# Performance work log

Measured on AMD Instinct MI355X. Metric: run time of the kernel, lower is better.

## Reference

```python
import jax, jax.numpy as jnp
import numpy as np

B, S, E, H, DK = 4, 1024, 1024, 16, 64
FF = 2048
SCALE = int(np.sqrt(DK))  # source uses int(np.sqrt(keySize)) = 8
EPS = 1e-5


def _mha(x_kv, x_q, Wq, Wk, Wv, Wo, mask):
    # Wq/Wk/Wv: [H, E, DK]; Wo: [H*DK, E]
    k = jnp.einsum('bse,hed->hbsd', x_kv, Wk)   # [H,B,S,DK]
    v = jnp.einsum('bse,hed->hbsd', x_kv, Wv)
    q = jnp.einsum('bse,hed->hbsd', x_q, Wq)
    # source does keys.reshape(B, DK, S) -- a RAW reshape, not a transpose
    kR = k.reshape(H, B, DK, S)
    scores = jnp.einsum('hbsd,hbdt->hbst', q, kR)  # [H,B,S,S]
    if mask is not None:
        scores = scores + mask  # mask added BEFORE the scale divide, as in source
    att = jax.nn.softmax(scores / SCALE, axis=-1)
    out = jnp.einsum('hbst,hbtd->hbsd', att, v)    # [H,B,S,DK]
    # source stacks heads then does a RAW reshape [H,B,S,DK] -> [B,S,DK*H]
    out = out.reshape(B, S, DK * H)
    return out @ Wo  # [B,S,E]


def _layernorm2d(x, w, b):
    # LayerNorm over last two dims (S, E) with affine params [S, E]
    m = jnp.mean(x, axis=(-2, -1), keepdims=True)
    v = jnp.var(x, axis=(-2, -1), keepdims=True)
    return (x - m) * jax.lax.rsqrt(v + EPS) * w + b


def setup_inputs() -> dict:
    key = jax.random.key(0)
    ks = jax.random.split(key, 24)
    u = lambda k, shp: jax.random.uniform(k, shp, dtype=jnp.float32)  # weights ~ U(0,1) as in source
    inp = {
        'inputRes': jax.random.normal(ks[0], (B, S, E), dtype=jnp.float32),
        'outputEncoding': jax.random.normal(ks[1], (B, S, E), dtype=jnp.float32),
        'Wq1': u(ks[2], (H, E, DK)), 'Wk1': u(ks[3], (H, E, DK)), 'Wv1': u(ks[4], (H, E, DK)),
        'Wo1': u(ks[5], (H * DK, E)),
        'Wq2': u(ks[6], (H, E, DK)), 'Wk2': u(ks[7], (H, E, DK)), 'Wv2': u(ks[8], (H, E, DK)),
        'Wo2': u(ks[9], (H * DK, E)),
        'ln1_w': jnp.ones((S, E), jnp.float32), 'ln1_b': jnp.zeros((S, E), jnp.float32),
        'ln2_w': jnp.ones((S, E), jnp.float32), 'ln2_b': jnp.zeros((S, E), jnp.float32),
        'ln3_w': jnp.ones((S, E), jnp.float32), 'ln3_b': jnp.zeros((S, E), jnp.float32),
        'W1': jax.random.normal(ks[10], (S, FF), dtype=jnp.float32) * (1.0 / np.sqrt(S)),
        'b1': jnp.zeros((FF,), jnp.float32),
        'W2': jax.random.normal(ks[11], (FF, S), dtype=jnp.float32) * (1.0 / np.sqrt(FF)),
        'b2': jnp.zeros((S,), jnp.float32),
    }
    return inp


def reference(inputRes, outputEncoding, Wq1, Wk1, Wv1, Wo1, Wq2, Wk2, Wv2, Wo2,
              ln1_w, ln1_b, ln2_w, ln2_b, ln3_w, ln3_b, W1, b1, W2, b2):
    # causal mask: row i has 0 for j<=i, -inf for j>i
    idx = jnp.arange(S)
    mask = jnp.where(idx[None, :] <= idx[:, None], 0.0, -jnp.inf).astype(jnp.float32)

    # masked self-attention + residual + LN1
    att = _mha(outputEncoding, outputEncoding, Wq1, Wk1, Wv1, Wo1, mask)
    att_norm = _layernorm2d(att + outputEncoding, ln1_w, ln1_b)

    # cross-attention (K,V from inputRes; Q from att_norm) + residual to outputEncoding + LN2
    att2 = _mha(inputRes, att_norm, Wq2, Wk2, Wv2, Wo2, None)
    att2_norm = _layernorm2d(att2 + outputEncoding, ln2_w, ln2_b)

    # FFN over the sequence dim via RAW reshape (B,S,E)->(B,E,S), as in source
    norm_res = att2_norm.reshape(B, E, S)
    fc = jax.nn.relu(norm_res @ W1 + b1) @ W2 + b2  # [B,E,S]
    fc = fc.reshape(B, S, E)

    return _layernorm2d(fc + att2_norm, ln3_w, ln3_b)
```

## Files before the change

kernel.cpp:

```cpp
#include <hip/hip_runtime.h>
#include <cstdint>
#include <cstddef>


#define DI __device__ __forceinline__
#define MFMA __builtin_amdgcn_mfma_f32_16x16x32_bf16

typedef short s8v __attribute__((ext_vector_type(8)));
typedef float f4v __attribute__((ext_vector_type(4)));
typedef unsigned u4v __attribute__((ext_vector_type(4)));

DI float bf2f(short u){
  union { unsigned int i; float f; } v;
  v.i = ((unsigned int)(unsigned short)u) << 16;
  return v.f;
}
DI short f2bf(float f){
  union { float f; unsigned int i; } v; v.f = f;
  unsigned int x = v.i;
  return (short)((x + 0x7fffu + ((x >> 16) & 1u)) >> 16);
}
DI unsigned pack2(short hi, short lo){
  return ((unsigned)(unsigned short)lo << 16) | (unsigned)(unsigned short)hi;
}
DI unsigned packf(float val){
  short hi = f2bf(val);
  return pack2(hi, f2bf(val - bf2f(hi)));
}
DI void gload16(const void* g, void* l){
  __builtin_amdgcn_global_load_lds(
      (const __attribute__((address_space(1))) unsigned*)g,
      (__attribute__((address_space(3))) unsigned*)l, 16, 0, 0);
}

struct SplitP { const float* src[2]; short* hi[2]; short* lo[2]; };

__launch_bounds__(256)
__global__ void splitall_k(SplitP sp){
  const int t = blockIdx.y;
  int i = (blockIdx.x * 256 + threadIdx.x) << 2;
  float4 v = *(const float4*)(sp.src[t] + i);
  float xs[4] = {v.x, v.y, v.z, v.w};
  short h[4], l[4];
  #pragma unroll
  for (int c = 0; c < 4; c++){
    h[c] = f2bf(xs[c]);
    l[c] = f2bf(xs[c] - bf2f(h[c]));
  }
  *(short4*)(sp.hi[t] + i) = make_short4(h[0], h[1], h[2], h[3]);
  *(short4*)(sp.lo[t] + i) = make_short4(l[0], l[1], l[2], l[3]);
}

struct TransP {
  const float* src[10];
  short* oh[10]; short* ol[10];
  int Kd[10]; int Nd[10]; int qkv[10]; int ntiles[10];
};

__launch_bounds__(256)
__global__ void transall_k(TransP tp){
  const int t = blockIdx.y;
  const int tile = blockIdx.x;
  if (tile >= tp.ntiles[t]) return;
  const int K = tp.Kd[t], N = tp.Nd[t];
  const int ncols = N >> 6;
  const int n0 = (tile % ncols) << 6, k0 = (tile / ncols) << 6;
  __shared__ float Ld[64 * 65];
  const int tid = threadIdx.x;
  const int row = tid >> 2, c16 = (tid & 3) << 4;
  const float* s = tp.src[t];
  size_t base;
  if (tp.qkv[t]) base = ((size_t)(n0 >> 6) << 16) + ((size_t)(k0 + row) << 6) + c16;
  else           base = (size_t)(k0 + row) * N + n0 + c16;
  #pragma unroll
  for (int j4 = 0; j4 < 4; j4++){
    float4 v = *(const float4*)(s + base + (j4 << 2));
    int c = row * 65 + c16 + (j4 << 2);
    Ld[c] = v.x; Ld[c + 1] = v.y; Ld[c + 2] = v.z; Ld[c + 3] = v.w;
  }
  __syncthreads();
  const int n = tid >> 2;
  s8v h0, h1, l0, l1;
  #pragma unroll
  for (int j = 0; j < 8; j++){
    float a = Ld[(c16 + j) * 65 + n];
    float b = Ld[(c16 + 8 + j) * 65 + n];
    short ha = f2bf(a), hb = f2bf(b);
    h0[j] = ha; l0[j] = f2bf(a - bf2f(ha));
    h1[j] = hb; l1[j] = f2bf(b - bf2f(hb));
  }
  size_t ob = (size_t)(n0 + n) * K + k0 + c16;
  *(s8v*)(tp.oh[t] + ob)     = h0;
  *(s8v*)(tp.oh[t] + ob + 8) = h1;
  *(s8v*)(tp.ol[t] + ob)     = l0;
  *(s8v*)(tp.ol[t] + ob + 8) = l1;
}

struct GemmP {
  const short* Ah; const short* Al; int lda;
  const short* Bh; const short* Bl; int ldb;
  int K; int N;
  const float* xres; const float* bias;
  float* outf;
  short* o1h; short* o1l;
  unsigned* p1; unsigned* p2; unsigned* p3;
};

template<int TM, int EPI, int TERMS>
__launch_bounds__(512, 2)
__global__ void gemm_k(GemmP p){
  constexpr int NG = (TERMS == 3) ? (TM / 64 + 2) : (TM / 128 + 2);
  constexpr int WM = TM >> 6;
  constexpr int NB = 128 / (8 / WM) / 16;
  __shared__ short AhL[3][TM * 32];
  __shared__ short AlL[3][(TERMS == 3) ? TM * 32 : 8];
  __shared__ short BhL[3][128 * 32];
  __shared__ short BlL[3][128 * 32];
  const int tid = threadIdx.x;
  const int L = tid & 63, w = tid >> 6;
  const int lr = L & 15, lg = L >> 4;
  const int mo = (w & (WM - 1)) << 6;
  const int no = (w / WM) * (NB << 4);

  const int gx = gridDim.x, gy = gridDim.y;
  const int f = blockIdx.y * gx + blockIdx.x;
  const int j = f >> 3;
  const int jm = j / gx;
  const int mb = (f & 7) * (gy >> 3) + jm;
  const int nb = j - jm * gx;
  const int m0 = mb * TM, n0 = nb << 7;

  const int lrow4 = L >> 2, lq = L & 3;

  int aoff[4], boff[NB];
  #pragma unroll
  for (int mi = 0; mi < 4; mi++){
    int r = mo + (mi << 4) + lr;
    aoff[mi] = (r << 5) + ((lg ^ ((r >> 1) & 3)) << 3);
  }
  #pragma unroll
  for (int ni = 0; ni < NB; ni++){
    int n = no + (ni << 4) + lr;
    boff[ni] = (n << 5) + ((lg ^ ((n >> 1) & 3)) << 3);
  }

  f4v acc[4][NB];
  #pragma unroll
  for (int i = 0; i < 4; i++)
    #pragma unroll
    for (int jj = 0; jj < NB; jj++)
      #pragma unroll
      for (int r = 0; r < 4; r++) acc[i][jj][r] = 0.0f;

  const int nkt = p.K >> 5;

  auto stage1 = [&](int tile, int slot, int i){
    const int k0 = tile << 5;
    int base_c = (i << 9) + (w << 6);
    const short* plane; short* lds; int row0; int ld; int pc;
    if (base_c < TM * 4){
      pc = base_c; plane = p.Ah; lds = &AhL[slot][0]; row0 = m0; ld = p.lda;
    } else if (TERMS == 3 && base_c < TM * 8){
      pc = base_c - TM * 4; plane = p.Al; lds = &AlL[slot][0]; row0 = m0; ld = p.lda;
    } else {
      int pc2 = base_c - (TERMS == 3 ? TM * 8 : TM * 4);
      if (pc2 < 512){ pc = pc2; plane = p.Bh; lds = &BhL[slot][0]; }
      else          { pc = pc2 - 512; plane = p.Bl; lds = &BlL[slot][0]; }
      row0 = n0; ld = p.ldb;
    }
    int rl = (pc >> 2) + lrow4;
    int sc = (lq ^ ((rl >> 1) & 3)) << 3;
    gload16(plane + (size_t)(row0 + rl) * ld + k0 + sc, lds + (pc << 3));
  };

  #pragma unroll
  for (int i = 0; i < NG; i++) stage1(0, 0, i);
  #pragma unroll
  for (int i = 0; i < NG; i++) stage1(1, 1, i);

  for (int kt = 0; kt < nkt; kt++){
    const int cur = kt % 3;
    const int nt = kt + 2 < nkt ? kt + 2 : nkt - 1;
    const int nslot = (kt + 2) % 3;
    asm volatile("s_waitcnt vmcnt(%0)\n\ts_barrier" :: "i"(NG) : "memory");

    s8v a_h[4], b_h[NB];
    #pragma unroll
    for (int mi = 0; mi < 4; mi++) a_h[mi] = *(const s8v*)&AhL[cur][aoff[mi]];
    #pragma unroll
    for (int ni = 0; ni < NB; ni++) b_h[ni] = *(const s8v*)&BhL[cur][boff[ni]];
    stage1(nt, nslot, 0);
    stage1(nt, nslot, 1);
    __builtin_amdgcn_s_barrier();
    __builtin_amdgcn_s_setprio(1);
    #pragma unroll
    for (int ni = 0; ni < NB; ni++)
      #pragma unroll
      for (int mi = 0; mi < 4; mi++)
        acc[mi][ni] = MFMA(a_h[mi], b_h[ni], acc[mi][ni], 0, 0, 0);
    __builtin_amdgcn_s_setprio(0);
    __builtin_amdgcn_s_barrier();

    s8v b_l[NB];
    #pragma unroll
    for (int ni = 0; ni < NB; ni++) b_l[ni] = *(const s8v*)&BlL[cur][boff[ni]];
    if (NG > 2) stage1(nt, nslot, 2);
    if (NG > 3) stage1(nt, nslot, 3);
    __builtin_amdgcn_s_barrier();
    __builtin_amdgcn_s_setprio(1);
    #pragma unroll
    for (int ni = 0; ni < NB; ni++)
      #pragma unroll
      for (int mi = 0; mi < 4; mi++)
        acc[mi][ni] = MFMA(a_h[mi], b_l[ni], acc[mi][ni], 0, 0, 0);
    __builtin_amdgcn_s_setprio(0);

    if (TERMS == 3){
      __builtin_amdgcn_s_barrier();
      s8v a_l[4];
      #pragma unroll
      for (int mi = 0; mi < 4; mi++) a_l[mi] = *(const s8v*)&AlL[cur][aoff[mi]];
      if (NG > 4) stage1(nt, nslot, 4);
      if (NG > 5) stage1(nt, nslot, 5);
      __builtin_amdgcn_s_barrier();
      __builtin_amdgcn_s_setprio(1);
      #pragma unroll
      for (int ni = 0; ni < NB; ni++)
        #pragma unroll
        for (int mi = 0; mi < 4; mi++)
          acc[mi][ni] = MFMA(a_l[mi], b_h[ni], acc[mi][ni], 0, 0, 0);
      __builtin_amdgcn_s_setprio(0);
    }
  }

  #pragma unroll
  for (int mi = 0; mi < 4; mi++){
    #pragma unroll
    for (int ni = 0; ni < NB; ni++){
      #pragma unroll
      for (int r = 0; r < 4; r++){
        float val = acc[mi][ni][r];
        int m = m0 + mo + (mi << 4) + (lg << 2) + r;
        int n = n0 + no + (ni << 4) + lr;
        if (EPI == 2){
          size_t o = (size_t)m * p.N + n;
          p.outf[o] = val + p.xres[o];
        } else if (EPI == 4){
          p.outf[(size_t)m * p.N + n] = val + p.bias[n];
        } else if (EPI == 3){
          float x = val + p.bias[n];
          x = x > 0.0f ? x : 0.0f;
          size_t o = (size_t)m * p.N + n;
          short hi = f2bf(x);
          p.o1h[o] = hi;
          p.o1l[o] = f2bf(x - bf2f(hi));
        } else {
          int seg = (EPI == 0) ? 0 : (n >> 10);
          int n1 = (EPI == 0) ? n : (n & 1023);
          int kind = (EPI == 0) ? 0 : (EPI == 6 ? seg : seg + 1);
          int b = m >> 10, s = m & 1023, hh = n1 >> 6, d = n1 & 63;
          size_t hb16 = (size_t)((hh << 2) | b) << 16;
          size_t dst;
          if (kind == 0)      dst = hb16 + ((size_t)s << 6) + d;
          else if (kind == 1) dst = hb16 + ((size_t)(((s & 15) << 6) | d) << 6) + (s >> 4);
          else                dst = hb16 + ((size_t)d << 10) + s;
          unsigned* dp = (EPI == 0) ? p.p1
                       : (EPI == 6) ? (seg == 0 ? p.p1 : (seg == 1 ? p.p2 : p.p3))
                                    : (seg == 0 ? p.p1 : p.p2);
          dp[dst] = packf(val);
        }
      }
    }
  }
}

template<int CAUSAL>
__launch_bounds__(256, 2)
__global__ void flash_k(const unsigned* __restrict__ qpk,
                        const unsigned* __restrict__ kpk,
                        const unsigned* __restrict__ vpk,
                        short* __restrict__ ohi_g, short* __restrict__ olo_g){
  __shared__ short Kt[2][64*72];
  __shared__ short Vt[2][64*72];
  __shared__ unsigned Ps[2][4][16*68];
  const int tid = threadIdx.x, L = tid & 63, w = tid >> 6;
  const int lr = L & 15, lg = L >> 4;
  const int flat = blockIdx.x + (blockIdx.y << 3);
  const int hb = ((flat & 7) << 3) | ((flat >> 3) & 7);
  const int sp = flat >> 6;
  const int h = hb >> 2, b = hb & 3;
  const size_t hbo = (size_t)hb << 16;
  const float NEG_INF = -__builtin_inff();
  int qt[2]; qt[0] = sp; qt[1] = CAUSAL ? (15 - sp) : (sp + 8);

  s8v qfh[2][2], qfl[2][2];
  #pragma unroll
  for (int st = 0; st < 2; st++){
    const unsigned* qg = qpk + hbo + (size_t)((qt[st] << 6) + (w << 4) + lr) * 64 + (lg << 3);
    #pragma unroll
    for (int ks = 0; ks < 2; ks++){
      u4v p0 = *(const u4v*)(qg + (ks << 5));
      u4v p1 = *(const u4v*)(qg + (ks << 5) + 4);
      #pragma unroll
      for (int jj = 0; jj < 4; jj++){
        qfh[st][ks][jj]     = (short)(p0[jj] & 0xffffu);
        qfl[st][ks][jj]     = (short)(p0[jj] >> 16);
        qfh[st][ks][4 + jj] = (short)(p1[jj] & 0xffffu);
        qfl[st][ks][4 + jj] = (short)(p1[jj] >> 16);
      }
    }
  }

  f4v o[2][4];
  float mprev[2][4], lsum[2][4];
  #pragma unroll
  for (int st = 0; st < 2; st++){
    #pragma unroll
    for (int ni = 0; ni < 4; ni++)
      #pragma unroll
      for (int r = 0; r < 4; r++) o[st][ni][r] = 0.0f;
    #pragma unroll
    for (int r = 0; r < 4; r++){ mprev[st][r] = NEG_INF; lsum[st][r] = 0.0f; }
  }

  const int ntt = CAUSAL ? (qt[1] + 1) : 16;
  for (int ti = 0; ti < ntt; ti++){
    const int t0 = ti << 6;
    const bool actA = !(CAUSAL && ti > qt[0]);
    __syncthreads();
    {
      const int row = tid >> 2, col = (tid & 3) << 4;
      const unsigned* kg = kpk + hbo + (size_t)(t0 + row) * 64 + col;
      const unsigned* vg = vpk + hbo + ((size_t)row << 10) + t0 + col;
      unsigned kb[16], vb[16];
      #pragma unroll
      for (int j4 = 0; j4 < 4; j4++){
        *(u4v*)&kb[j4 << 2] = *(const u4v*)(kg + (j4 << 2));
        *(u4v*)&vb[j4 << 2] = *(const u4v*)(vg + (j4 << 2));
      }
      s8v kh0, kh1, kl0, kl1, vh0, vh1, vl0, vl1;
      #pragma unroll
      for (int jj = 0; jj < 8; jj++){
        kh0[jj] = (short)(kb[jj] & 0xffffu);      kl0[jj] = (short)(kb[jj] >> 16);
        kh1[jj] = (short)(kb[8 + jj] & 0xffffu);  kl1[jj] = (short)(kb[8 + jj] >> 16);
        vh0[jj] = (short)(vb[jj] & 0xffffu);      vl0[jj] = (short)(vb[jj] >> 16);
        vh1[jj] = (short)(vb[8 + jj] & 0xffffu);  vl1[jj] = (short)(vb[8 + jj] >> 16);
      }
      const int lb = row * 72 + col;
      *(s8v*)&Kt[0][lb] = kh0;  *(s8v*)&Kt[0][lb + 8] = kh1;
      *(s8v*)&Kt[1][lb] = kl0;  *(s8v*)&Kt[1][lb + 8] = kl1;
      *(s8v*)&Vt[0][lb] = vh0;  *(s8v*)&Vt[0][lb + 8] = vh1;
      *(s8v*)&Vt[1][lb] = vl0;  *(s8v*)&Vt[1][lb + 8] = vl1;
    }
    __syncthreads();

    f4v sa[2][4];
    #pragma unroll
    for (int st = 0; st < 2; st++)
      #pragma unroll
      for (int ni = 0; ni < 4; ni++)
        #pragma unroll
        for (int r = 0; r < 4; r++) sa[st][ni][r] = 0.0f;
    #pragma unroll
    for (int ks = 0; ks < 2; ks++){
      const int kb = (ks << 5) + (lg << 3);
      #pragma unroll
      for (int ni = 0; ni < 4; ni++){
        const int tl = (ni << 4) + lr;
        s8v kbh = *(const s8v*)&Kt[0][tl * 72 + kb];
        s8v kbl = *(const s8v*)&Kt[1][tl * 72 + kb];
        if (actA){
          sa[0][ni] = MFMA(qfh[0][ks], kbh, sa[0][ni], 0, 0, 0);
          sa[0][ni] = MFMA(qfh[0][ks], kbl, sa[0][ni], 0, 0, 0);
          sa[0][ni] = MFMA(qfl[0][ks], kbh, sa[0][ni], 0, 0, 0);
        }
        sa[1][ni] = MFMA(qfh[1][ks], kbh, sa[1][ni], 0, 0, 0);
        sa[1][ni] = MFMA(qfh[1][ks], kbl, sa[1][ni], 0, 0, 0);
        sa[1][ni] = MFMA(qfl[1][ks], kbh, sa[1][ni], 0, 0, 0);
      }
    }

    #pragma unroll
    for (int st = 0; st < 2; st++){
      if (st == 0 && !actA) continue;
      const int s0w = (qt[st] << 6) + (w << 4);
      const bool diag = CAUSAL && (ti == qt[st]);
      float tm[4] = {NEG_INF, NEG_INF, NEG_INF, NEG_INF};
      #pragma unroll
      for (int ni = 0; ni < 4; ni++)
        #pragma unroll
        for (int r = 0; r < 4; r++){
          float v = sa[st][ni][r] * 0.125f;
          if (diag){
            int tg = t0 + (ni << 4) + lr;
            int sg = s0w + (lg << 2) + r;
            if (tg > sg) v = NEG_INF;
          }
          sa[st][ni][r] = v;
          tm[r] = fmaxf(tm[r], v);
        }
      #pragma unroll
      for (int off = 1; off < 16; off <<= 1)
        #pragma unroll
        for (int r = 0; r < 4; r++) tm[r] = fmaxf(tm[r], __shfl_xor(tm[r], off, 16));
      float alpha[4], psum[4];
      #pragma unroll
      for (int r = 0; r < 4; r++){
        float mn = fmaxf(mprev[st][r], tm[r]);
        alpha[r] = __expf(mprev[st][r] - mn);
        mprev[st][r] = mn;
        psum[r] = 0.0f;
      }
      #pragma unroll
      for (int ni = 0; ni < 4; ni++)
        #pragma unroll
        for (int r = 0; r < 4; r++){
          float pv = __expf(sa[st][ni][r] - mprev[st][r]);
          sa[st][ni][r] = pv;
          psum[r] += pv;
        }
      #pragma unroll
      for (int off = 1; off < 16; off <<= 1)
        #pragma unroll
        for (int r = 0; r < 4; r++) psum[r] += __shfl_xor(psum[r], off, 16);
      #pragma unroll
      for (int r = 0; r < 4; r++) lsum[st][r] = lsum[st][r] * alpha[r] + psum[r];
      #pragma unroll
      for (int ni = 0; ni < 4; ni++)
        #pragma unroll
        for (int r = 0; r < 4; r++) o[st][ni][r] *= alpha[r];
      #pragma unroll
      for (int ni = 0; ni < 4; ni++)
        #pragma unroll
        for (int r = 0; r < 4; r++){
          int prow = (lg << 2) + r, pcol = (ni << 4) + lr;
          Ps[st][w][prow * 68 + pcol] = packf(sa[st][ni][r]);
        }
    }

    #pragma unroll
    for (int ks = 0; ks < 2; ks++){
      const int kb = (ks << 5) + (lg << 3);
      s8v ph[2], pl[2];
      #pragma unroll
      for (int st = 0; st < 2; st++){
        if (st == 0 && !actA) continue;
        u4v p0 = *(const u4v*)&Ps[st][w][lr * 68 + kb];
        u4v p1 = *(const u4v*)&Ps[st][w][lr * 68 + kb + 4];
        #pragma unroll
        for (int jj = 0; jj < 4; jj++){
          ph[st][jj]     = (short)(p0[jj] & 0xffffu);  pl[st][jj]     = (short)(p0[jj] >> 16);
          ph[st][4 + jj] = (short)(p1[jj] & 0xffffu);  pl[st][4 + jj] = (short)(p1[jj] >> 16);
        }
      }
      #pragma unroll
      for (int ni = 0; ni < 4; ni++){
        const int d = (ni << 4) + lr;
        s8v vbh = *(const s8v*)&Vt[0][d * 72 + kb];
        s8v vbl = *(const s8v*)&Vt[1][d * 72 + kb];
        if (actA){
          o[0][ni] = MFMA(ph[0], vbh, o[0][ni], 0, 0, 0);
          o[0][ni] = MFMA(ph[0], vbl, o[0][ni], 0, 0, 0);
          o[0][ni] = MFMA(pl[0], vbh, o[0][ni], 0, 0, 0);
        }
        o[1][ni] = MFMA(ph[1], vbh, o[1][ni], 0, 0, 0);
        o[1][ni] = MFMA(ph[1], vbl, o[1][ni], 0, 0, 0);
        o[1][ni] = MFMA(pl[1], vbh, o[1][ni], 0, 0, 0);
      }
    }
  }

  #pragma unroll
  for (int st = 0; st < 2; st++){
    const int s0w = (qt[st] << 6) + (w << 4);
    #pragma unroll
    for (int ni = 0; ni < 4; ni++){
      #pragma unroll
      for (int r = 0; r < 4; r++){
        float val = o[st][ni][r] / lsum[st][r];
        int s = s0w + (lg << 2) + r;
        int d = (ni << 4) + lr;
        int s2i = ((h & 3) << 8) | (b << 6) | (s >> 4);
        int c   = ((s & 15) << 6) | d;
        size_t dst = ((size_t)(h >> 2) << 20) + ((size_t)s2i << 10) + c;
        short hi = f2bf(val);
        ohi_g[dst] = hi;
        olo_g[dst] = f2bf(val - bf2f(hi));
      }
    }
  }
}

__launch_bounds__(256)
__global__ void ln_partial_k(const float* s1, const float* s2, float2* part){
  const int tid = threadIdx.x, L = tid & 63, w = tid >> 6;
  const int b = blockIdx.y, j = blockIdx.x;
  const size_t base = ((size_t)b << 20) + ((size_t)j << 13) + ((size_t)tid << 2);
  float sum = 0.0f, ss = 0.0f;
  #pragma unroll
  for (int i = 0; i < 8; i++){
    size_t idx = base + ((size_t)i << 10);
    float4 v = *(const float4*)(s1 + idx);
    if (s2){
      float4 u = *(const float4*)(s2 + idx);
      v.x += u.x; v.y += u.y; v.z += u.z; v.w += u.w;
    }
    sum += v.x + v.y + v.z + v.w;
    ss  += v.x*v.x + v.y*v.y + v.z*v.z + v.w*v.w;
  }
  #pragma unroll
  for (int off = 1; off < 64; off <<= 1){
    sum += __shfl_xor(sum, off, 64);
    ss  += __shfl_xor(ss,  off, 64);
  }
  __shared__ float red[4][2];
  if (L == 0){ red[w][0] = sum; red[w][1] = ss; }
  __syncthreads();
  if (tid == 0){
    float s_ = red[0][0] + red[1][0] + red[2][0] + red[3][0];
    float q_ = red[0][1] + red[1][1] + red[2][1] + red[3][1];
    part[b * 128 + j] = make_float2(s_, q_);
  }
}

__launch_bounds__(64)
__global__ void ln_final_k(const float2* part, float2* stats){
  const int b = blockIdx.x, t = threadIdx.x;
  float2 a = part[b * 128 + t], c = part[b * 128 + 64 + t];
  float sum = a.x + c.x, ss = a.y + c.y;
  #pragma unroll
  for (int off = 1; off < 64; off <<= 1){
    sum += __shfl_xor(sum, off, 64);
    ss  += __shfl_xor(ss,  off, 64);
  }
  if (t == 0){
    float mean = sum * (1.0f / 1048576.0f);
    float var  = ss  * (1.0f / 1048576.0f) - mean * mean;
    stats[b] = make_float2(mean, rsqrtf(var + 1e-5f));
  }
}

template<int MODE>
__launch_bounds__(256)
__global__ void ln_apply_k(const float* s1, const float* s2,
                           const float* wgt, const float* bias,
                           const float2* stats,
                           float* dstf, short* dsta, short* dstb){
  const int tid = threadIdx.x;
  const size_t base = ((size_t)blockIdx.x << 11) + ((size_t)tid << 2);
  #pragma unroll
  for (int i = 0; i < 2; i++){
    size_t idx = base + ((size_t)i << 10);
    int b = (int)(idx >> 20);
    float2 st = stats[b];
    float4 x = *(const float4*)(s1 + idx);
    if (s2){
      float4 u = *(const float4*)(s2 + idx);
      x.x += u.x; x.y += u.y; x.z += u.z; x.w += u.w;
    }
    unsigned wi = (unsigned)(idx & 1048575u);
    float4 wv = *(const float4*)(wgt + wi);
    float4 bv = *(const float4*)(bias + wi);
    float xv[4] = {x.x, x.y, x.z, x.w};
    float wvv[4] = {wv.x, wv.y, wv.z, wv.w};
    float bvv[4] = {bv.x, bv.y, bv.z, bv.w};
    float yv[4];
    #pragma unroll
    for (int c = 0; c < 4; c++)
      yv[c] = (xv[c] - st.x) * st.y * wvv[c] + bvv[c];
    if (MODE == 0 || MODE == 1){
      short h[4], l[4];
      #pragma unroll
      for (int c = 0; c < 4; c++){
        h[c] = f2bf(yv[c]);
        l[c] = f2bf(yv[c] - bf2f(h[c]));
      }
      *(short4*)(dsta + idx) = make_short4(h[0], h[1], h[2], h[3]);
      *(short4*)(dstb + idx) = make_short4(l[0], l[1], l[2], l[3]);
      if (MODE == 1)
        *(float4*)(dstf + idx) = make_float4(yv[0], yv[1], yv[2], yv[3]);
    } else {
      *(float4*)(dstf + idx) = make_float4(yv[0], yv[1], yv[2], yv[3]);
    }
  }
}

extern "C" void kernel_launch(void* const* d_in, const int* in_sizes, int n_in,
                              void* d_out, int out_size, void* d_ws, size_t ws_size,
                              hipStream_t stream){
  const float* IRf = (const float*)d_in[0];
  const float* OEf = (const float*)d_in[1];
  const float* Wq1f = (const float*)d_in[2];
  const float* Wk1f = (const float*)d_in[3];
  const float* Wv1f = (const float*)d_in[4];
  const float* Wo1f = (const float*)d_in[5];
  const float* Wq2f = (const float*)d_in[6];
  const float* Wk2f = (const float*)d_in[7];
  const float* Wv2f = (const float*)d_in[8];
  const float* Wo2f = (const float*)d_in[9];
  const float* ln1w = (const float*)d_in[10];
  const float* ln1b = (const float*)d_in[11];
  const float* ln2w = (const float*)d_in[12];
  const float* ln2b = (const float*)d_in[13];
  const float* ln3w = (const float*)d_in[14];
  const float* ln3b = (const float*)d_in[15];
  const float* W1f = (const float*)d_in[16];
  const float* b1f = (const float*)d_in[17];
  const float* W2f = (const float*)d_in[18];
  const float* b2f = (const float*)d_in[19];
  float* dout = (float*)d_out;

  char* ws = (char*)d_ws;
  const size_t MB = (size_t)1 << 20;
  short* OEh = (short*)(ws + 0*MB),  *OEl = (short*)(ws + 8*MB);
  short* IRh = (short*)(ws + 16*MB), *IRl = (short*)(ws + 24*MB);
  short* QKV1t_h = (short*)(ws + 32*MB), *QKV1t_l = (short*)(ws + 38*MB);
  short* Wo1t_h  = (short*)(ws + 44*MB), *Wo1t_l  = (short*)(ws + 46*MB);
  short* Q2t_h   = (short*)(ws + 48*MB), *Q2t_l   = (short*)(ws + 50*MB);
  short* KV2t_h  = (short*)(ws + 52*MB), *KV2t_l  = (short*)(ws + 56*MB);
  short* Wo2t_h  = (short*)(ws + 60*MB), *Wo2t_l  = (short*)(ws + 62*MB);
  short* W1t_h   = (short*)(ws + 64*MB), *W1t_l   = (short*)(ws + 68*MB);
  short* W2t_h   = (short*)(ws + 72*MB), *W2t_l   = (short*)(ws + 76*MB);
  unsigned* q_pk = (unsigned*)(ws + 80*MB);
  unsigned* k_pk = (unsigned*)(ws + 96*MB);
  unsigned* v_pk = (unsigned*)(ws + 112*MB);
  short* outr_h = (short*)(ws + 128*MB), *outr_l = (short*)(ws + 136*MB);
  float* resid = (float*)(ws + 144*MB);
  short* attn_h = (short*)(ws + 160*MB), *attn_l = (short*)(ws + 168*MB);
  float* att2n_f = (float*)(ws + 176*MB);
  short* hid_h = (short*)(ws + 80*MB);
  short* hid_l = (short*)(ws + 96*MB);
  float* fc    = (float*)(ws + 112*MB);
  short* a2n_h = (short*)(ws + 160*MB);
  short* a2n_l = (short*)(ws + 168*MB);
  float2* part  = (float2*)(ws + 192*MB);
  float2* stats = (float2*)(ws + 192*MB + 65536);

  dim3 blk(256), blkg(512);

  SplitP sp;
  sp.src[0] = OEf; sp.hi[0] = OEh; sp.lo[0] = OEl;
  sp.src[1] = IRf; sp.hi[1] = IRh; sp.lo[1] = IRl;
  splitall_k<<<dim3(4096, 2), blk, 0, stream>>>(sp);

  TransP tp;
  const float* tsrc[10] = {Wq1f, Wk1f, Wv1f, Wo1f, Wq2f, Wk2f, Wv2f, Wo2f, W1f, W2f};
  short* toh[10] = {QKV1t_h, QKV1t_h + (1<<20), QKV1t_h + (2<<20), Wo1t_h,
                    Q2t_h, KV2t_h, KV2t_h + (1<<20), Wo2t_h, W1t_h, W2t_h};
  short* tol[10] = {QKV1t_l, QKV1t_l + (1<<20), QKV1t_l + (2<<20), Wo1t_l,
                    Q2t_l, KV2t_l, KV2t_l + (1<<20), Wo2t_l, W1t_l, W2t_l};
  int tK[10]   = {1024,1024,1024,1024,1024,1024,1024,1024,1024,2048};
  int tN[10]   = {1024,1024,1024,1024,1024,1024,1024,1024,2048,1024};
  int tq[10]   = {1,1,1,0,1,1,1,0,0,0};
  int tt[10]   = {256,256,256,256,256,256,256,256,512,512};
  for (int i = 0; i < 10; i++){
    tp.src[i] = tsrc[i]; tp.oh[i] = toh[i]; tp.ol[i] = tol[i];
    tp.Kd[i] = tK[i]; tp.Nd[i] = tN[i]; tp.qkv[i] = tq[i]; tp.ntiles[i] = tt[i];
  }
  transall_k<<<dim3(512, 10), blk, 0, stream>>>(tp);

  GemmP p{};

  p = {OEh, OEl, 1024, QKV1t_h, QKV1t_l, 1024, 1024, 3072, nullptr, nullptr,
       nullptr, nullptr, nullptr, q_pk, k_pk, v_pk};
  gemm_k<256,6,3><<<dim3(24, 16), blkg, 0, stream>>>(p);
  flash_k<1><<<dim3(8, 64), blk, 0, stream>>>(q_pk, k_pk, v_pk, outr_h, outr_l);
  p = {outr_h, outr_l, 1024, Wo1t_h, Wo1t_l, 1024, 1024, 1024, OEf, nullptr,
       resid, nullptr, nullptr, nullptr, nullptr, nullptr};
  gemm_k<128,2,3><<<dim3(8, 32), blkg, 0, stream>>>(p);
  ln_partial_k<<<dim3(128, 4), blk, 0, stream>>>(resid, nullptr, part);
  ln_final_k<<<dim3(4), dim3(64), 0, stream>>>(part, stats);
  ln_apply_k<0><<<dim3(2048), blk, 0, stream>>>(resid, nullptr, ln1w, ln1b, stats, nullptr, attn_h, attn_l);

  p = {attn_h, attn_l, 1024, Q2t_h, Q2t_l, 1024, 1024, 1024, nullptr, nullptr,
       nullptr, nullptr, nullptr, q_pk, nullptr, nullptr};
  gemm_k<128,0,3><<<dim3(8, 32), blkg, 0, stream>>>(p);
  p = {IRh, IRl, 1024, KV2t_h, KV2t_l, 1024, 1024, 2048, nullptr, nullptr,
       nullptr, nullptr, nullptr, k_pk, v_pk, nullptr};
  gemm_k<256,7,3><<<dim3(16, 16), blkg, 0, stream>>>(p);
  flash_k<0><<<dim3(8, 64), blk, 0, stream>>>(q_pk, k_pk, v_pk, outr_h, outr_l);
  p = {outr_h, outr_l, 1024, Wo2t_h, Wo2t_l, 1024, 1024, 1024, OEf, nullptr,
       resid, nullptr, nullptr, nullptr, nullptr, nullptr};
  gemm_k<128,2,3><<<dim3(8, 32), blkg, 0, stream>>>(p);
  ln_partial_k<<<dim3(128, 4), blk, 0, stream>>>(resid, nullptr, part);
  ln_final_k<<<dim3(4), dim3(64), 0, stream>>>(part, stats);
  ln_apply_k<1><<<dim3(2048), blk, 0, stream>>>(resid, nullptr, ln2w, ln2b, stats, att2n_f, a2n_h, a2n_l);

  p = {a2n_h, a2n_l, 1024, W1t_h, W1t_l, 1024, 1024, 2048, nullptr, b1f,
       nullptr, hid_h, hid_l, nullptr, nullptr, nullptr};
  gemm_k<256,3,2><<<dim3(16, 16), blkg, 0, stream>>>(p);
  p = {hid_h, hid_l, 2048, W2t_h, W2t_l, 2048, 2048, 1024, nullptr, b2f,
       fc, nullptr, nullptr, nullptr, nullptr, nullptr};
  gemm_k<128,4,2><<<dim3(8, 32), blkg, 0, stream>>>(p);
  ln_partial_k<<<dim3(128, 4), blk, 0, stream>>>(fc, att2n_f, part);
  ln_final_k<<<dim3(4), dim3(64), 0, stream>>>(part, stats);
  ln_apply_k<2><<<dim3(2048), blk, 0, stream>>>(fc, att2n_f, ln3w, ln3b, stats, dout, nullptr, nullptr);
}
```

Before: 738.6 us.

## Restructure split-bf16 GEMM pipeline: double-buffer hi planes, stream Bl from registers

The GEMM main loop drops from a three-stage LDS ring holding all four hi/lo planes to a two-stage ring for only the hi planes. The B low plane now loads straight from global memory into registers, and the A low plane sits in a single-buffered LDS tile refilled after a barrier. The Bh·Al and Al·Bh MFMAs are interleaved, and per-phase barriers and setprio calls are removed. The smaller LDS footprint lets launch bounds rise to 4 blocks per CU, and two GEMMs switch from 256-row to 128-row tiles with doubled grids. The trade-offs are less prefetch depth, uncoalesced direct-to-register Bl loads, and extra register pressure under the tighter occupancy bound.

Measured after the change: 903.6 us. +22.3%, slower.

```diff
diff --git a/kernel.cpp b/kernel.cpp
--- a/kernel.cpp
+++ b/kernel.cpp
@@ -107,15 +107,15 @@
 };
 
 template<int TM, int EPI, int TERMS>
-__launch_bounds__(512, 2)
+__launch_bounds__(512, 4)
 __global__ void gemm_k(GemmP p){
-  constexpr int NG = (TERMS == 3) ? (TM / 64 + 2) : (TM / 128 + 2);
   constexpr int WM = TM >> 6;
   constexpr int NB = 128 / (8 / WM) / 16;
-  __shared__ short AhL[3][TM * 32];
-  __shared__ short AlL[3][(TERMS == 3) ? TM * 32 : 8];
-  __shared__ short BhL[3][128 * 32];
-  __shared__ short BlL[3][128 * 32];
+  constexpr int NH = TM / 128 + 1;
+  constexpr int NA = (TERMS == 3) ? TM / 128 : 0;
+  __shared__ short AhL[2][TM * 32];
+  __shared__ short BhL[2][128 * 32];
+  __shared__ short AlL[(TERMS == 3) ? TM * 32 : 8];
   const int tid = threadIdx.x;
   const int L = tid & 63, w = tid >> 6;
   const int lr = L & 15, lg = L >> 4;
@@ -154,83 +154,82 @@
 
   const int nkt = p.K >> 5;
 
-  auto stage1 = [&](int tile, int slot, int i){
+  auto stage_hi = [&](int tile, int slot, int i){
     const int k0 = tile << 5;
     int base_c = (i << 9) + (w << 6);
     const short* plane; short* lds; int row0; int ld; int pc;
     if (base_c < TM * 4){
       pc = base_c; plane = p.Ah; lds = &AhL[slot][0]; row0 = m0; ld = p.lda;
-    } else if (TERMS == 3 && base_c < TM * 8){
-      pc = base_c - TM * 4; plane = p.Al; lds = &AlL[slot][0]; row0 = m0; ld = p.lda;
     } else {
-      int pc2 = base_c - (TERMS == 3 ? TM * 8 : TM * 4);
-      if (pc2 < 512){ pc = pc2; plane = p.Bh; lds = &BhL[slot][0]; }
-      else          { pc = pc2 - 512; plane = p.Bl; lds = &BlL[slot][0]; }
-      row0 = n0; ld = p.ldb;
+      pc = base_c - TM * 4; plane = p.Bh; lds = &BhL[slot][0]; row0 = n0; ld = p.ldb;
     }
     int rl = (pc >> 2) + lrow4;
     int sc = (lq ^ ((rl >> 1) & 3)) << 3;
     gload16(plane + (size_t)(row0 + rl) * ld + k0 + sc, lds + (pc << 3));
   };
-
-  #pragma unroll
-  for (int i = 0; i < NG; i++) stage1(0, 0, i);
-  #pragma unroll
-  for (int i = 0; i < NG; i++) stage1(1, 1, i);
+  auto stage_al = [&](int tile, int i){
+    const int k0 = tile << 5;
+    int pc = (i << 9) + (w << 6);
+    int rl = (pc >> 2) + lrow4;
+    int sc = (lq ^ ((rl >> 1) & 3)) << 3;
+    gload16(p.Al + (size_t)(m0 + rl) * p.lda + k0 + sc, &AlL[pc << 3]);
+  };
+
+  s8v bl[NB];
+  auto bl_load = [&](int tile){
+    #pragma unroll
+    for (int ni = 0; ni < NB; ni++)
+      bl[ni] = *(const s8v*)(p.Bl + (size_t)(n0 + no + (ni << 4) + lr) * p.ldb
+                             + (tile << 5) + (lg << 3));
+  };
+
+  #pragma unroll
+  for (int i = 0; i < NH; i++) stage_hi(0, 0, i);
+  if (TERMS == 3){
+    #pragma unroll
+    for (int i = 0; i < NA; i++) stage_al(0, i);
+  }
+  bl_load(0);
 
   for (int kt = 0; kt < nkt; kt++){
-    const int cur = kt % 3;
-    const int nt = kt + 2 < nkt ? kt + 2 : nkt - 1;
-    const int nslot = (kt + 2) % 3;
-    asm volatile("s_waitcnt vmcnt(%0)\n\ts_barrier" :: "i"(NG) : "memory");
-
-    s8v a_h[4], b_h[NB];
+    const int cur = kt & 1;
+    const int nt = kt + 1 < nkt ? kt + 1 : nkt - 1;
+    asm volatile("s_waitcnt vmcnt(%0)\n\ts_barrier" :: "i"(NB) : "memory");
+    #pragma unroll
+    for (int i = 0; i < NH; i++) stage_hi(nt, cur ^ 1, i);
+
+    s8v a_h[4], b_h[NB], a_l[4];
     #pragma unroll
     for (int mi = 0; mi < 4; mi++) a_h[mi] = *(const s8v*)&AhL[cur][aoff[mi]];
     #pragma unroll
     for (int ni = 0; ni < NB; ni++) b_h[ni] = *(const s8v*)&BhL[cur][boff[ni]];
-    stage1(nt, nslot, 0);
-    stage1(nt, nslot, 1);
-    __builtin_amdgcn_s_barrier();
-    __builtin_amdgcn_s_setprio(1);
+    if (TERMS == 3){
+      #pragma unroll
+      for (int mi = 0; mi < 4; mi++) a_l[mi] = *(const s8v*)&AlL[aoff[mi]];
+    }
+
     #pragma unroll
     for (int ni = 0; ni < NB; ni++)
       #pragma unroll
       for (int mi = 0; mi < 4; mi++)
         acc[mi][ni] = MFMA(a_h[mi], b_h[ni], acc[mi][ni], 0, 0, 0);
-    __builtin_amdgcn_s_setprio(0);
-    __builtin_amdgcn_s_barrier();
-
-    s8v b_l[NB];
-    #pragma unroll
-    for (int ni = 0; ni < NB; ni++) b_l[ni] = *(const s8v*)&BlL[cur][boff[ni]];
-    if (NG > 2) stage1(nt, nslot, 2);
-    if (NG > 3) stage1(nt, nslot, 3);
-    __builtin_amdgcn_s_barrier();
-    __builtin_amdgcn_s_setprio(1);
     #pragma unroll
     for (int ni = 0; ni < NB; ni++)
       #pragma unroll
-      for (int mi = 0; mi < 4; mi++)
-        acc[mi][ni] = MFMA(a_h[mi], b_l[ni], acc[mi][ni], 0, 0, 0);
-    __builtin_amdgcn_s_setprio(0);
+      for (int mi = 0; mi < 4; mi++){
+        acc[mi][ni] = MFMA(a_h[mi], bl[ni], acc[mi][ni], 0, 0, 0);
+        if (TERMS == 3)
+          acc[mi][ni] = MFMA(a_l[mi], b_h[ni], acc[mi][ni], 0, 0, 0);
+      }
 
     if (TERMS == 3){
-      __builtin_amdgcn_s_barrier();
-      s8v a_l[4];
-      #pragma unroll
-      for (int mi = 0; mi < 4; mi++) a_l[mi] = *(const s8v*)&AlL[cur][aoff[mi]];
-      if (NG > 4) stage1(nt, nslot, 4);
-      if (NG > 5) stage1(nt, nslot, 5);
-      __builtin_amdgcn_s_barrier();
-      __builtin_amdgcn_s_setprio(1);
-      #pragma unroll
-      for (int ni = 0; ni < NB; ni++)
-        #pragma unroll
-        for (int mi = 0; mi < 4; mi++)
-          acc[mi][ni] = MFMA(a_l[mi], b_h[ni], acc[mi][ni], 0, 0, 0);
-      __builtin_amdgcn_s_setprio(0);
-    }
+      asm volatile("s_barrier" ::: "memory");
+      #pragma unroll
+      for (int i = 0; i < NA; i++) stage_al(nt, i);
+    } else {
+      asm volatile("" ::: "memory");
+    }
+    bl_load(nt);
   }
 
   #pragma unroll
@@ -677,7 +676,7 @@
   gemm_k<128,0,3><<<dim3(8, 32), blkg, 0, stream>>>(p);
   p = {IRh, IRl, 1024, KV2t_h, KV2t_l, 1024, 1024, 2048, nullptr, nullptr,
        nullptr, nullptr, nullptr, k_pk, v_pk, nullptr};
-  gemm_k<256,7,3><<<dim3(16, 16), blkg, 0, stream>>>(p);
+  gemm_k<128,7,3><<<dim3(16, 32), blkg, 0, stream>>>(p);
   flash_k<0><<<dim3(8, 64), blk, 0, stream>>>(q_pk, k_pk, v_pk, outr_h, outr_l);
   p = {outr_h, outr_l, 1024, Wo2t_h, Wo2t_l, 1024, 1024, 1024, OEf, nullptr,
        resid, nullptr, nullptr, nullptr, nullptr, nullptr};
@@ -688,7 +687,7 @@
 
   p = {a2n_h, a2n_l, 1024, W1t_h, W1t_l, 1024, 1024, 2048, nullptr, b1f,
        nullptr, hid_h, hid_l, nullptr, nullptr, nullptr};
-  gemm_k<256,3,2><<<dim3(16, 16), blkg, 0, stream>>>(p);
+  gemm_k<128,3,2><<<dim3(16, 32), blkg, 0, stream>>>(p);
   p = {hid_h, hid_l, 2048, W2t_h, W2t_l, 2048, 2048, 1024, nullptr, b2f,
        fc, nullptr, nullptr, nullptr, nullptr, nullptr};
   gemm_k<128,4,2><<<dim3(8, 32), blkg, 0, stream>>>(p);
```
